# Optimization experiments

Hardware: AMD Instinct MI355X
Metric: run time of the kernel (lower is better)

Reference implementation:

```python
import jax, jax.numpy as jnp
import numpy as np
import math

B, S, D, H = 2, 2048, 1024, 16
HD = D // H  # head dim = 64


def setup_inputs() -> dict:
    key = jax.random.key(0)
    ks = jax.random.split(key, 8)
    scale = 1.0 / math.sqrt(D)
    return {
        "x": jax.random.normal(ks[0], (B, S, D), dtype=jnp.float32),
        "mask": jax.random.randint(ks[1], (B, S, S), 0, 2).astype(bool),
        "Wq": jax.random.normal(ks[2], (D, D), dtype=jnp.float32) * scale,
        "bq": jax.random.normal(ks[3], (D,), dtype=jnp.float32) * 0.01,
        "Wk": jax.random.normal(ks[4], (D, D), dtype=jnp.float32) * scale,
        "bk": jax.random.normal(ks[5], (D,), dtype=jnp.float32) * 0.01,
        "Wv": jax.random.normal(ks[6], (D, D), dtype=jnp.float32) * scale,
        "bv": jax.random.normal(ks[7], (D,), dtype=jnp.float32) * 0.01,
    }


def reference(x, mask, Wq, bq, Wk, bk, Wv, bv):
    # Linear projections (weights stored as [in, out])
    q = x @ Wq + bq  # [B,S,D]
    k = x @ Wk + bk
    v = x @ Wv + bv
    # split heads -> [B,H,S,HD]
    q = q.reshape(B, S, H, HD).transpose(0, 2, 1, 3)
    k = k.reshape(B, S, H, HD).transpose(0, 2, 1, 3)
    v = v.reshape(B, S, H, HD).transpose(0, 2, 1, 3)
    scores = jnp.einsum("bhqd,bhkd->bhqk", q, k) / jnp.sqrt(jnp.float32(HD))
    # Faithful to the source: masked_fill_(mask, -inf) is immediately
    # overwritten by masked_fill_(mask, 0), so masked positions end up 0
    # BEFORE the softmax (a quirk of the original module).
    scores = jnp.where(mask[:, None, :, :], 0.0, scores)
    attn = jax.nn.softmax(scores, axis=-1)  # dropout=0.0 (eval)
    out = jnp.einsum("bhqk,bhkd->bhqd", attn, v)
    return out.transpose(0, 2, 1, 3).reshape(B, S, D)
```

## Files before the change

### kernel.cpp

```cpp
#include <hip/hip_runtime.h>
#include <cstdint>
#include <cstddef>

static constexpr int B_ = 2, S_ = 2048, D_ = 1024, H_ = 16, HD_ = 64;

typedef float f32x4 __attribute__((ext_vector_type(4)));
typedef short bf16x8 __attribute__((ext_vector_type(8)));

__device__ __forceinline__ unsigned short f2bf(float f) {
    union { float f; unsigned int u; } v; v.f = f;
    unsigned int r = v.u + 0x7FFFu + ((v.u >> 16) & 1u);
    return (unsigned short)(r >> 16);
}

__device__ __forceinline__ unsigned pack2bf(float a, float b) {
    union { float f; unsigned u; } va, vb; va.f = a; vb.f = b;
    unsigned ra = va.u + 0x7FFFu + ((va.u >> 16) & 1u);
    unsigned rb = vb.u + 0x7FFFu + ((vb.u >> 16) & 1u);
    return __builtin_amdgcn_perm(rb, ra, 0x07060302u);
}

__device__ __forceinline__ void gload_lds16(const void* g, void* l) {
    __builtin_amdgcn_global_load_lds(
        (const __attribute__((address_space(1))) void*)g,
        (__attribute__((address_space(3))) void*)l, 16, 0, 0);
}

__global__ __launch_bounds__(256)
void prep(const float* __restrict__ x, unsigned short* __restrict__ xo,
          const int* __restrict__ m, unsigned char* __restrict__ mo,
          const float* __restrict__ Wq, const float* __restrict__ Wk,
          const float* __restrict__ Wv, unsigned short* __restrict__ wt) {
    __shared__ unsigned short Ts[64][72];
    const int bid = blockIdx.x, t = threadIdx.x;
    if (bid < 2048) {
        size_t i = ((size_t)bid * 256 + t) * 8;
        float4 a = *(const float4*)(x + i);
        float4 c = *(const float4*)(x + i + 4);
        uint4 r;
        r.x = pack2bf(a.x, a.y); r.y = pack2bf(a.z, a.w);
        r.z = pack2bf(c.x, c.y); r.w = pack2bf(c.z, c.w);
        *(uint4*)(xo + i) = r;
    } else if (bid < 4096) {
        size_t i = ((size_t)(bid - 2048) * 256 + t) * 16;
        uint4 r;
        unsigned w[4];
        #pragma unroll
        for (int g = 0; g < 4; ++g) {
            int4 v = *(const int4*)(m + i + g * 4);
            w[g] = (v.x ? 0xFFu : 0u) | (v.y ? 0xFF00u : 0u) |
                   (v.z ? 0xFF0000u : 0u) | (v.w ? 0xFF000000u : 0u);
        }
        r.x = w[0]; r.y = w[1]; r.z = w[2]; r.w = w[3];
        *(uint4*)(mo + i) = r;
    } else {
        const int tid = bid - 4096;
        const int mat = tid >> 8, tile = tid & 255;
        const float* __restrict__ W = (mat == 0) ? Wq : (mat == 1) ? Wk : Wv;
        unsigned short* __restrict__ o = wt + (size_t)mat * D_ * D_;
        const int n0 = (tile & 15) * 64, k0 = (tile >> 4) * 64;
        {
            const int nl = t & 63, kb = t >> 6;
            #pragma unroll
            for (int i = 0; i < 16; ++i) {
                int k = kb + i * 4;
                Ts[nl][k] = f2bf(W[(size_t)(k0 + k) * D_ + n0 + nl]);
            }
        }
        __syncthreads();
        {
            const int kl = t & 63, nb = t >> 6;
            #pragma unroll
            for (int i = 0; i < 16; ++i) {
                int n = nb + i * 4;
                o[(size_t)(n0 + n) * D_ + k0 + kl] = Ts[n][kl];
            }
        }
    }
}

__global__ __launch_bounds__(512)
void qkv_gemm(const unsigned short* __restrict__ xb, const unsigned short* __restrict__ wt,
              const float* __restrict__ bq, const float* __restrict__ bk,
              const float* __restrict__ bv,
              unsigned short* __restrict__ qo, unsigned short* __restrict__ ko,
              unsigned short* __restrict__ vto) {
    const int bx = blockIdx.x;
    const int by = blockIdx.y;
    const int mat = bx >> 3;
    const int ncol0 = (bx & 7) * 128;
    const float* __restrict__ bias = (mat == 0) ? bq : (mat == 1) ? bk : bv;
    const unsigned short* __restrict__ Wm = wt + (size_t)mat * D_ * D_;

    __shared__ unsigned short As[2][128 * 32];
    __shared__ unsigned short Bs[2][128 * 32];

    const int t = threadIdx.x;
    const int w = t >> 6, lane = t & 63;
    const int l15 = lane & 15, quad = lane >> 4;
    const int mw = (w >> 2) * 64, nw = (w & 3) * 32;
    const int rowBase = by * 128;

    const int r16 = lane >> 2;
    const int sslot = lane & 3;
    const int sg = (sslot ^ ((r16 >> 1) & 3)) * 8;
    const int srow = w * 16 + r16;
    const int rcol = (quad ^ ((l15 >> 1) & 3)) * 8;

    f32x4 acc[4][2] = {};

    gload_lds16(xb + (size_t)(rowBase + srow) * D_ + sg, &As[0][w * 16 * 32]);
    gload_lds16(Wm + (size_t)(ncol0 + srow) * D_ + sg, &Bs[0][w * 16 * 32]);

    for (int it = 0; it < 32; ++it) {
        const int cur = it & 1;
        __syncthreads();
        if (it + 1 < 32) {
            const int ktn = (it + 1) * 32;
            gload_lds16(xb + (size_t)(rowBase + srow) * D_ + ktn + sg,
                        &As[cur ^ 1][w * 16 * 32]);
            gload_lds16(Wm + (size_t)(ncol0 + srow) * D_ + ktn + sg,
                        &Bs[cur ^ 1][w * 16 * 32]);
        }

        bf16x8 a[4], b[2];
        #pragma unroll
        for (int i = 0; i < 4; ++i)
            a[i] = *(const bf16x8*)&As[cur][(mw + i * 16 + l15) * 32 + rcol];
        #pragma unroll
        for (int j = 0; j < 2; ++j)
            b[j] = *(const bf16x8*)&Bs[cur][(nw + j * 16 + l15) * 32 + rcol];
        #pragma unroll
        for (int i = 0; i < 4; ++i)
            #pragma unroll
            for (int j = 0; j < 2; ++j)
                acc[i][j] = __builtin_amdgcn_mfma_f32_16x16x32_bf16(a[i], b[j], acc[i][j], 0, 0, 0);
    }

    if (mat < 2) {
        unsigned short* __restrict__ O = (mat == 0) ? qo : ko;
        const float osc = (mat == 0) ? 0.18033688011112443f : 1.0f;
        #pragma unroll
        for (int j = 0; j < 2; ++j) {
            const int col = ncol0 + nw + j * 16 + l15;
            const float bb = bias[col];
            #pragma unroll
            for (int i = 0; i < 4; ++i)
                #pragma unroll
                for (int r = 0; r < 4; ++r) {
                    const int m = rowBase + mw + i * 16 + quad * 4 + r;
                    O[(size_t)m * D_ + col] = f2bf((acc[i][j][r] + bb) * osc);
                }
        }
    } else {
        #pragma unroll
        for (int j = 0; j < 2; ++j) {
            const int col = ncol0 + nw + j * 16 + l15;
            const float bb = bias[col];
            const int hh = col >> 6, hd = col & 63;
            #pragma unroll
            for (int i = 0; i < 4; ++i) {
                const int m0 = rowBase + mw + i * 16 + quad * 4;
                const int bg = m0 >> 11, s0 = m0 & 2047;
                ushort4 pk;
                pk.x = f2bf(acc[i][j][0] + bb);
                pk.y = f2bf(acc[i][j][1] + bb);
                pk.z = f2bf(acc[i][j][2] + bb);
                pk.w = f2bf(acc[i][j][3] + bb);
                *(ushort4*)&vto[(((size_t)bg * H_ + hh) * HD_ + hd) * S_ + s0] = pk;
            }
        }
    }
}

__global__ __launch_bounds__(512, 4)
void attn_mfma(const unsigned short* __restrict__ qmat,
               const unsigned short* __restrict__ kmat,
               const unsigned short* __restrict__ vtg,
               const unsigned char* __restrict__ msk,
               float* __restrict__ opart, float* __restrict__ lspart) {
    const int h = blockIdx.x, yy = blockIdx.y, b = blockIdx.z;
    const int qt = yy >> 1, half = yy & 1;
    const int t = threadIdx.x, w = t >> 6, lane = t & 63;
    const int l15 = lane & 15, quad = lane >> 4;
    const int q0 = qt * 128;

    __shared__ __align__(16) char smem[49152];
    unsigned short* const Ksm = (unsigned short*)smem;
    unsigned short* const Vsm = (unsigned short*)(smem + 16384);
    unsigned short* const Psm = (unsigned short*)(smem + 32768);

    const size_t bh = (size_t)b * S_ * D_ + (size_t)h * HD_;
    const unsigned short* __restrict__ qp = qmat + bh;
    const unsigned short* __restrict__ kp = kmat + bh + (size_t)half * 1024 * D_;
    const unsigned short* __restrict__ vp = vtg + ((size_t)b * H_ + h) * HD_ * S_ + half * 1024;
    const unsigned char* __restrict__ mb = msk + (size_t)b * S_ * S_ + half * 1024;

    const int rs = lane >> 3, sslot = lane & 7;
    const int sg = (sslot ^ rs) * 8;
    const int srow = w * 8 + rs;

    const int qs = w >> 1;
    const int kw = (w & 1) * 32;
    const int kst = w & 1;
    const int sw7 = l15 & 7;

    bf16x8 qfr[2][2];
    #pragma unroll
    for (int nt = 0; nt < 2; ++nt)
        #pragma unroll
        for (int dk = 0; dk < 2; ++dk)
            qfr[nt][dk] = *(const bf16x8*)(qp +
                (size_t)(q0 + qs * 32 + nt * 16 + l15) * D_ + dk * 32 + quad * 8);

    f32x4 accO[2][4] = {};
    f32x4 lsA[2] = {};
    bf16x8 ones;
    #pragma unroll
    for (int i = 0; i < 8; ++i) ones[i] = (short)0x3F80;

    gload_lds16(kp + (size_t)srow * D_ + sg, Ksm + w * 8 * 64);
    gload_lds16(vp + (size_t)srow * S_ + sg, Vsm + w * 8 * 64);

#define ATTN_STEP(IT, CUR)                                                     \
    do {                                                                       \
        const int kt = (IT) * 64;                                              \
        __syncthreads();                                                       \
        unsigned mu[2][2];                                                     \
        _Pragma("unroll")                                                      \
        for (int nt = 0; nt < 2; ++nt) {                                       \
            const unsigned char* __restrict__ mrow =                           \
                mb + (size_t)(q0 + qs * 32 + nt * 16 + l15) * S_ + kt + kw;    \
            mu[nt][0] = *(const unsigned*)(mrow + quad * 4);                   \
            mu[nt][1] = *(const unsigned*)(mrow + 16 + quad * 4);              \
        }                                                                      \
        if ((IT) + 1 < 16) {                                                   \
            const int ktn = kt + 64;                                           \
            gload_lds16(kp + (size_t)(ktn + srow) * D_ + sg,                   \
                        Ksm + ((CUR) ^ 1) * 4096 + w * 8 * 64);                \
            gload_lds16(vp + (size_t)srow * S_ + ktn + sg,                     \
                        Vsm + ((CUR) ^ 1) * 4096 + w * 8 * 64);                \
        }                                                                      \
        f32x4 sc[2][2] = {};                                                   \
        _Pragma("unroll")                                                      \
        for (int dk = 0; dk < 2; ++dk) {                                       \
            bf16x8 kfr[2];                                                     \
            _Pragma("unroll")                                                  \
            for (int mt = 0; mt < 2; ++mt) {                                   \
                const int R = kw + mt * 16 + l15;                              \
                kfr[mt] = *(const bf16x8*)&Ksm[(CUR) * 4096 + R * 64 +         \
                                               (((dk * 4 + quad) ^ sw7) * 8)]; \
            }                                                                  \
            __builtin_amdgcn_s_setprio(1);                                     \
            _Pragma("unroll")                                                  \
            for (int nt = 0; nt < 2; ++nt)                                     \
                _Pragma("unroll")                                              \
                for (int mt = 0; mt < 2; ++mt)                                 \
                    sc[nt][mt] = __builtin_amdgcn_mfma_f32_16x16x32_bf16(      \
                        kfr[mt], qfr[nt][dk], sc[nt][mt], 0, 0, 0);            \
            __builtin_amdgcn_s_setprio(0);                                     \
        }                                                                      \
        _Pragma("unroll")                                                      \
        for (int nt = 0; nt < 2; ++nt) {                                       \
            const int qr = qs * 32 + nt * 16 + l15;                            \
            _Pragma("unroll")                                                  \
            for (int mt = 0; mt < 2; ++mt) {                                   \
                const int mtg = kst * 2 + mt;                                  \
                unsigned p0 = pack2bf(__builtin_amdgcn_exp2f(sc[nt][mt][0]),   \
                                      __builtin_amdgcn_exp2f(sc[nt][mt][1]));  \
                unsigned p1 = pack2bf(__builtin_amdgcn_exp2f(sc[nt][mt][2]),   \
                                      __builtin_amdgcn_exp2f(sc[nt][mt][3]));  \
                const unsigned m0 =                                            \
                    __builtin_amdgcn_perm(0u, mu[nt][mt], 0x01010000u);        \
                const unsigned m1 =                                            \
                    __builtin_amdgcn_perm(0u, mu[nt][mt], 0x03030202u);        \
                p0 = (m0 & 0x3F803F80u) | (~m0 & p0);                          \
                p1 = (m1 & 0x3F803F80u) | (~m1 & p1);                          \
                uint2 pk2; pk2.x = p0; pk2.y = p1;                             \
                *(uint2*)((char*)Psm + qr * 128 +                              \
                          (((2 * mtg + (quad >> 1)) ^ sw7) * 16) +             \
                          (quad & 1) * 8) = pk2;                               \
            }                                                                  \
        }                                                                      \
        {                                                                      \
            bf16x8 vfr[4];                                                     \
            _Pragma("unroll")                                                  \
            for (int dt = 0; dt < 4; ++dt) {                                   \
                const int R = dt * 16 + l15;                                   \
                vfr[dt] = *(const bf16x8*)&Vsm[(CUR) * 4096 + R * 64 +         \
                                               (((kst * 4 + quad) ^ sw7) * 8)];\
            }                                                                  \
            _Pragma("unroll")                                                  \
            for (int nt = 0; nt < 2; ++nt) {                                   \
                const int qr = qs * 32 + nt * 16 + l15;                        \
                bf16x8 pfr = *(const bf16x8*)((const char*)Psm + qr * 128 +    \
                                              (((kst * 4 + quad) ^ sw7) * 16));\
                __builtin_amdgcn_s_setprio(1);                                 \
                _Pragma("unroll")                                              \
                for (int dt = 0; dt < 4; ++dt)                                 \
                    accO[nt][dt] = __builtin_amdgcn_mfma_f32_16x16x32_bf16(    \
                        pfr, vfr[dt], accO[nt][dt], 0, 0, 0);                  \
                lsA[nt] = __builtin_amdgcn_mfma_f32_16x16x32_bf16(             \
                    pfr, ones, lsA[nt], 0, 0, 0);                              \
                __builtin_amdgcn_s_setprio(0);                                 \
            }                                                                  \
        }                                                                      \
    } while (0)

    for (int io = 0; io < 8; ++io) {
        ATTN_STEP(2 * io, 0);
        ATTN_STEP(2 * io + 1, 1);
    }
#undef ATTN_STEP

    __syncthreads();
    float* const Red = (float*)smem;
    if (w & 1) {
        #pragma unroll
        for (int nt = 0; nt < 2; ++nt) {
            const int pidx = ((qs * 2 + nt) * 64 + lane) * 20;
            #pragma unroll
            for (int dt = 0; dt < 4; ++dt)
                *(f32x4*)&Red[pidx + dt * 4] = accO[nt][dt];
            *(f32x4*)&Red[pidx + 16] = lsA[nt];
        }
    }
    __syncthreads();
    if (!(w & 1)) {
        float* __restrict__ op = opart +
            (((size_t)half * B_ + b) * S_ + q0) * D_ + (size_t)h * HD_;
        #pragma unroll
        for (int nt = 0; nt < 2; ++nt) {
            const int pidx = ((qs * 2 + nt) * 64 + lane) * 20;
            #pragma unroll
            for (int dt = 0; dt < 4; ++dt)
                accO[nt][dt] += *(const f32x4*)&Red[pidx + dt * 4];
            lsA[nt] += *(const f32x4*)&Red[pidx + 16];

            #pragma unroll
            for (int r = 0; r < 4; ++r) {
                const int row = qs * 32 + nt * 16 + quad * 4 + r;
                #pragma unroll
                for (int dt = 0; dt < 4; ++dt)
                    op[(size_t)row * D_ + dt * 16 + l15] = accO[nt][dt][r];
            }
            if (l15 == 0) {
                #pragma unroll
                for (int r = 0; r < 4; ++r) {
                    const int row = qs * 32 + nt * 16 + quad * 4 + r;
                    lspart[(((size_t)half * B_ + b) * H_ + h) * S_ + q0 + row] =
                        lsA[nt][r];
                }
            }
        }
    }
}

__global__ __launch_bounds__(256)
void attn_reduce(const float* __restrict__ Op, const float* __restrict__ Ls,
                 float* __restrict__ out) {
    const size_t i = ((size_t)blockIdx.x * 256 + threadIdx.x) * 4;
    const size_t HALF = (size_t)B_ * S_ * D_;
    float4 p0 = *(const float4*)(Op + i);
    float4 p1 = *(const float4*)(Op + HALF + i);
    const int rowg = (int)(i >> 10);
    const int col = (int)(i & 1023);
    const int b = rowg >> 11, row = rowg & 2047, h = col >> 6;
    const float l = Ls[((size_t)b * H_ + h) * S_ + row] +
                    Ls[((size_t)(B_ + b) * H_ + h) * S_ + row];
    const float inv = 1.0f / l;
    float4 o;
    o.x = (p0.x + p1.x) * inv;
    o.y = (p0.y + p1.y) * inv;
    o.z = (p0.z + p1.z) * inv;
    o.w = (p0.w + p1.w) * inv;
    *(float4*)(out + i) = o;
}

extern "C" void kernel_launch(void* const* d_in, const int* in_sizes, int n_in,
                              void* d_out, int out_size, void* d_ws, size_t ws_size,
                              hipStream_t stream) {
    (void)in_sizes; (void)n_in; (void)out_size; (void)ws_size;
    const float* x    = (const float*)d_in[0];
    const int*   mask = (const int*)d_in[1];
    const float* Wq   = (const float*)d_in[2];
    const float* bq   = (const float*)d_in[3];
    const float* Wk   = (const float*)d_in[4];
    const float* bk   = (const float*)d_in[5];
    const float* Wv   = (const float*)d_in[6];
    const float* bv   = (const float*)d_in[7];
    float* out = (float*)d_out;

    const size_t M1 = (size_t)1024 * 1024;
    unsigned short* xb  = (unsigned short*)d_ws;
    unsigned short* wtb = xb + 4 * M1;
    unsigned short* qb  = wtb + 3 * M1;
    unsigned short* kb  = qb + 4 * M1;
    unsigned short* vtb = kb + 4 * M1;
    unsigned char*  mk  = (unsigned char*)(vtb + 4 * M1);
    float* opart = (float*)(mk + 8 * M1);
    float* lspart = opart + 2 * (size_t)B_ * S_ * D_;

    prep<<<4864, 256, 0, stream>>>(x, xb, mask, mk, Wq, Wk, Wv, wtb);
    qkv_gemm<<<dim3(24, 32), 512, 0, stream>>>(xb, wtb, bq, bk, bv, qb, kb, vtb);
    attn_mfma<<<dim3(16, 32, 2), 512, 0, stream>>>(qb, kb, vtb, mk, opart, lspart);
    attn_reduce<<<4096, 256, 0, stream>>>(opart, lspart, out);
}
```

Before: 236.4 us.

## Drop split-K attention halves and triple-buffer K/V with explicit vmcnt waits

The attention kernel no longer splits the key range into two halves. Each block now walks all 2048 keys and normalises its output directly, which removes the partial-output buffers and the separate reduce kernel. The K/V staging moves from double to triple buffering, prefetching two tiles ahead, and the full __syncthreads is replaced by an inline s_waitcnt vmcnt plus s_barrier. The grid is halved to 512 blocks and LDS use grows to 64KB, which may cut occupancy and parallelism while saving the fp32 partial write/read traffic and one launch.

```diff
diff --git a/kernel.cpp b/kernel.cpp
--- a/kernel.cpp
+++ b/kernel.cpp
@@ -177,24 +177,22 @@
 void attn_mfma(const unsigned short* __restrict__ qmat,
                const unsigned short* __restrict__ kmat,
                const unsigned short* __restrict__ vtg,
-               const unsigned char* __restrict__ msk,
-               float* __restrict__ opart, float* __restrict__ lspart) {
-    const int h = blockIdx.x, yy = blockIdx.y, b = blockIdx.z;
-    const int qt = yy >> 1, half = yy & 1;
+               const unsigned char* __restrict__ msk, float* __restrict__ out) {
+    const int h = blockIdx.x, qt = blockIdx.y, b = blockIdx.z;
     const int t = threadIdx.x, w = t >> 6, lane = t & 63;
     const int l15 = lane & 15, quad = lane >> 4;
     const int q0 = qt * 128;
 
-    __shared__ __align__(16) char smem[49152];
+    __shared__ __align__(16) char smem[65536];
     unsigned short* const Ksm = (unsigned short*)smem;
-    unsigned short* const Vsm = (unsigned short*)(smem + 16384);
-    unsigned short* const Psm = (unsigned short*)(smem + 32768);
+    unsigned short* const Vsm = (unsigned short*)(smem + 24576);
+    unsigned short* const Psm = (unsigned short*)(smem + 49152);
 
     const size_t bh = (size_t)b * S_ * D_ + (size_t)h * HD_;
     const unsigned short* __restrict__ qp = qmat + bh;
-    const unsigned short* __restrict__ kp = kmat + bh + (size_t)half * 1024 * D_;
-    const unsigned short* __restrict__ vp = vtg + ((size_t)b * H_ + h) * HD_ * S_ + half * 1024;
-    const unsigned char* __restrict__ mb = msk + (size_t)b * S_ * S_ + half * 1024;
+    const unsigned short* __restrict__ kp = kmat + bh;
+    const unsigned short* __restrict__ vp = vtg + ((size_t)b * H_ + h) * HD_ * S_;
+    const unsigned char* __restrict__ mb = msk + (size_t)b * S_ * S_;
 
     const int rs = lane >> 3, sslot = lane & 7;
     const int sg = (sslot ^ rs) * 8;
@@ -221,11 +219,14 @@
 
     gload_lds16(kp + (size_t)srow * D_ + sg, Ksm + w * 8 * 64);
     gload_lds16(vp + (size_t)srow * S_ + sg, Vsm + w * 8 * 64);
-
-#define ATTN_STEP(IT, CUR)                                                     \
+    gload_lds16(kp + (size_t)(64 + srow) * D_ + sg, Ksm + 4096 + w * 8 * 64);
+    gload_lds16(vp + (size_t)srow * S_ + 64 + sg, Vsm + 4096 + w * 8 * 64);
+
+#define ATTN_STEP(IT, BUF, PRE, WAITN, DOPRE)                                  \
     do {                                                                       \
         const int kt = (IT) * 64;                                              \
-        __syncthreads();                                                       \
+        asm volatile("s_waitcnt vmcnt(%0)\n\ts_barrier"                        \
+                     :: "n"(WAITN) : "memory");                                \
         unsigned mu[2][2];                                                     \
         _Pragma("unroll")                                                      \
         for (int nt = 0; nt < 2; ++nt) {                                       \
@@ -234,12 +235,12 @@
             mu[nt][0] = *(const unsigned*)(mrow + quad * 4);                   \
             mu[nt][1] = *(const unsigned*)(mrow + 16 + quad * 4);              \
         }                                                                      \
-        if ((IT) + 1 < 16) {                                                   \
-            const int ktn = kt + 64;                                           \
+        if (DOPRE) {                                                           \
+            const int ktn = kt + 128;                                          \
             gload_lds16(kp + (size_t)(ktn + srow) * D_ + sg,                   \
-                        Ksm + ((CUR) ^ 1) * 4096 + w * 8 * 64);                \
+                        Ksm + (PRE) * 4096 + w * 8 * 64);                      \
             gload_lds16(vp + (size_t)srow * S_ + ktn + sg,                     \
-                        Vsm + ((CUR) ^ 1) * 4096 + w * 8 * 64);                \
+                        Vsm + (PRE) * 4096 + w * 8 * 64);                      \
         }                                                                      \
         f32x4 sc[2][2] = {};                                                   \
         _Pragma("unroll")                                                      \
@@ -248,7 +249,7 @@
             _Pragma("unroll")                                                  \
             for (int mt = 0; mt < 2; ++mt) {                                   \
                 const int R = kw + mt * 16 + l15;                              \
-                kfr[mt] = *(const bf16x8*)&Ksm[(CUR) * 4096 + R * 64 +         \
+                kfr[mt] = *(const bf16x8*)&Ksm[(BUF) * 4096 + R * 64 +         \
                                                (((dk * 4 + quad) ^ sw7) * 8)]; \
             }                                                                  \
             __builtin_amdgcn_s_setprio(1);                                     \
@@ -287,7 +288,7 @@
             _Pragma("unroll")                                                  \
             for (int dt = 0; dt < 4; ++dt) {                                   \
                 const int R = dt * 16 + l15;                                   \
-                vfr[dt] = *(const bf16x8*)&Vsm[(CUR) * 4096 + R * 64 +         \
+                vfr[dt] = *(const bf16x8*)&Vsm[(BUF) * 4096 + R * 64 +         \
                                                (((kst * 4 + quad) ^ sw7) * 8)];\
             }                                                                  \
             _Pragma("unroll")                                                  \
@@ -307,10 +308,16 @@
         }                                                                      \
     } while (0)
 
-    for (int io = 0; io < 8; ++io) {
-        ATTN_STEP(2 * io, 0);
-        ATTN_STEP(2 * io + 1, 1);
-    }
+    ATTN_STEP(0, 0, 2, 2, true);
+    ATTN_STEP(1, 1, 0, 6, true);
+    ATTN_STEP(2, 2, 1, 6, true);
+    for (int io = 1; io < 10; ++io) {
+        ATTN_STEP(3 * io + 0, 0, 2, 6, true);
+        ATTN_STEP(3 * io + 1, 1, 0, 6, true);
+        ATTN_STEP(3 * io + 2, 2, 1, 6, true);
+    }
+    ATTN_STEP(30, 0, 2, 6, false);
+    ATTN_STEP(31, 1, 0, 4, false);
 #undef ATTN_STEP
 
     __syncthreads();
@@ -327,8 +334,7 @@
     }
     __syncthreads();
     if (!(w & 1)) {
-        float* __restrict__ op = opart +
-            (((size_t)half * B_ + b) * S_ + q0) * D_ + (size_t)h * HD_;
+        float* __restrict__ ob = out + ((size_t)b * S_ + q0) * D_ + (size_t)h * HD_;
         #pragma unroll
         for (int nt = 0; nt < 2; ++nt) {
             const int pidx = ((qs * 2 + nt) * 64 + lane) * 20;
@@ -339,42 +345,14 @@
 
             #pragma unroll
             for (int r = 0; r < 4; ++r) {
+                const float inv = 1.0f / lsA[nt][r];
                 const int row = qs * 32 + nt * 16 + quad * 4 + r;
                 #pragma unroll
                 for (int dt = 0; dt < 4; ++dt)
-                    op[(size_t)row * D_ + dt * 16 + l15] = accO[nt][dt][r];
+                    ob[(size_t)row * D_ + dt * 16 + l15] = accO[nt][dt][r] * inv;
             }
-            if (l15 == 0) {
-                #pragma unroll
-                for (int r = 0; r < 4; ++r) {
-                    const int row = qs * 32 + nt * 16 + quad * 4 + r;
-                    lspart[(((size_t)half * B_ + b) * H_ + h) * S_ + q0 + row] =
-                        lsA[nt][r];
-                }
-            }
-        }
-    }
-}
-
-__global__ __launch_bounds__(256)
-void attn_reduce(const float* __restrict__ Op, const float* __restrict__ Ls,
-                 float* __restrict__ out) {
-    const size_t i = ((size_t)blockIdx.x * 256 + threadIdx.x) * 4;
-    const size_t HALF = (size_t)B_ * S_ * D_;
-    float4 p0 = *(const float4*)(Op + i);
-    float4 p1 = *(const float4*)(Op + HALF + i);
-    const int rowg = (int)(i >> 10);
-    const int col = (int)(i & 1023);
-    const int b = rowg >> 11, row = rowg & 2047, h = col >> 6;
-    const float l = Ls[((size_t)b * H_ + h) * S_ + row] +
-                    Ls[((size_t)(B_ + b) * H_ + h) * S_ + row];
-    const float inv = 1.0f / l;
-    float4 o;
-    o.x = (p0.x + p1.x) * inv;
-    o.y = (p0.y + p1.y) * inv;
-    o.z = (p0.z + p1.z) * inv;
-    o.w = (p0.w + p1.w) * inv;
-    *(float4*)(out + i) = o;
+        }
+    }
 }
 
 extern "C" void kernel_launch(void* const* d_in, const int* in_sizes, int n_in,
@@ -398,11 +376,8 @@
     unsigned short* kb  = qb + 4 * M1;
     unsigned short* vtb = kb + 4 * M1;
     unsigned char*  mk  = (unsigned char*)(vtb + 4 * M1);
-    float* opart = (float*)(mk + 8 * M1);
-    float* lspart = opart + 2 * (size_t)B_ * S_ * D_;
 
     prep<<<4864, 256, 0, stream>>>(x, xb, mask, mk, Wq, Wk, Wv, wtb);
     qkv_gemm<<<dim3(24, 32), 512, 0, stream>>>(xb, wtb, bq, bk, bv, qb, kb, vtb);
-    attn_mfma<<<dim3(16, 32, 2), 512, 0, stream>>>(qb, kb, vtb, mk, opart, lspart);
-    attn_reduce<<<4096, 256, 0, stream>>>(opart, lspart, out);
-}
+    attn_mfma<<<dim3(16, 16, 2), 512, 0, stream>>>(qb, kb, vtb, mk, out);
+}
```

Result: faster. 216.7 us (-8.4%).
